# Kernel tuning notes

Measured on AMD Instinct MI355X. Metric: run time of the kernel, lower is better.

The kernel has to match this reference:

```python
import jax, jax.numpy as jnp
import numpy as np

T, R, H, DK = 2, 3, 4, 32
IN_DIM, OUT_DIM = 128, 128
N = 50000
E = 400000
RELS = [(0, 1), (1, 0), (1, 1)]  # (src_type, dst_type) per relation


def setup_inputs() -> dict:
    key = jax.random.key(0)
    ks = jax.random.split(key, 24)
    lin_scale = float(np.sqrt(2.0 / (IN_DIM + OUT_DIM)))
    att_scale = float(np.sqrt(2.0 / (DK + DK)))
    inp = {
        'h0': jax.random.normal(ks[0], (N, IN_DIM), jnp.float32),
        'h1': jax.random.normal(ks[1], (N, IN_DIM), jnp.float32),
        'Wk': jax.random.normal(ks[2], (T, IN_DIM, OUT_DIM), jnp.float32) * lin_scale,
        'bk': jnp.zeros((T, OUT_DIM), jnp.float32),
        'Wq': jax.random.normal(ks[3], (T, IN_DIM, OUT_DIM), jnp.float32) * lin_scale,
        'bq': jnp.zeros((T, OUT_DIM), jnp.float32),
        'Wv': jax.random.normal(ks[4], (T, IN_DIM, OUT_DIM), jnp.float32) * lin_scale,
        'bv': jnp.zeros((T, OUT_DIM), jnp.float32),
        'Wa': jax.random.normal(ks[5], (T, OUT_DIM, OUT_DIM), jnp.float32) * lin_scale,
        'ba': jnp.zeros((T, OUT_DIM), jnp.float32),
        'rel_att': jax.random.normal(ks[6], (R, H, DK, DK), jnp.float32) * att_scale,
        'rel_msg': jax.random.normal(ks[7], (R, H, DK, DK), jnp.float32) * att_scale,
        'rel_pri': jnp.ones((R, H), jnp.float32),
        'skip': jnp.ones((T,), jnp.float32),
        'src0': jax.random.randint(ks[8], (E,), 0, N, jnp.int32),
        'dst0': jax.random.randint(ks[9], (E,), 0, N, jnp.int32),
        'src1': jax.random.randint(ks[10], (E,), 0, N, jnp.int32),
        'dst1': jax.random.randint(ks[11], (E,), 0, N, jnp.int32),
        'src2': jax.random.randint(ks[12], (E,), 0, N, jnp.int32),
        'dst2': jax.random.randint(ks[13], (E,), 0, N, jnp.int32),
    }
    return inp


def _hgt_forward(h0, h1, Wk, bk, Wq, bq, Wv, bv, Wa, ba,
                 rel_att, rel_msg, rel_pri, skip, edges):
    sqrt_dk = np.sqrt(DK).astype(np.float32)
    hs = [h0, h1]
    # per-type k/q/v projections, reshaped to [N, H, DK]
    k_all = [(hs[t] @ Wk[t] + bk[t]).reshape(-1, H, DK) for t in range(T)]
    q_all = [(hs[t] @ Wq[t] + bq[t]).reshape(-1, H, DK) for t in range(T)]
    v_all = [(hs[t] @ Wv[t] + bv[t]).reshape(-1, H, DK) for t in range(T)]
    agg = {0: [], 1: []}
    for r, (s, d) in enumerate(RELS):
        src, dst = edges[r]
        k = jnp.einsum('nhi,hij->nhj', k_all[s], rel_att[r])
        v = jnp.einsum('nhi,hij->nhj', v_all[s], rel_msg[r])
        q = q_all[d]
        # edge-wise dot-product attention score [E, H]
        score = jnp.einsum('ehd,ehd->eh', q[dst], k[src]) * rel_pri[r] / sqrt_dk
        # edge softmax normalized by destination node
        m = jax.ops.segment_max(score, dst, num_segments=N)
        e = jnp.exp(score - m[dst])
        z = jax.ops.segment_sum(e, dst, num_segments=N)
        a = e / z[dst]
        msg = v[src] * a[..., None]  # [E, H, DK]
        agg[d].append(jax.ops.segment_sum(msg, dst, num_segments=N))
    outs = []
    for t in range(T):
        tmean = agg[t][0]
        for extra in agg[t][1:]:
            tmean = tmean + extra
        tmean = tmean / jnp.float32(len(agg[t]))  # cross_reducer='mean'
        tt = tmean.reshape(-1, OUT_DIM)
        trans = tt @ Wa[t] + ba[t]  # dropout p=0 -> identity
        alpha = jax.nn.sigmoid(skip[t])
        outs.append(trans * alpha + hs[t] * (1.0 - alpha))
    return jnp.stack(outs)  # [T, N, OUT_DIM]


def reference(h0, h1, Wk, bk, Wq, bq, Wv, bv, Wa, ba,
              rel_att, rel_msg, rel_pri, skip,
              src0, dst0, src1, dst1, src2, dst2):
    edges = [(src0, dst0), (src1, dst1), (src2, dst2)]
    return _hgt_forward(h0, h1, Wk, bk, Wq, bq, Wv, bv, Wa, ba,
                        rel_att, rel_msg, rel_pri, skip, edges)
```

## Files before the change

### kernel.cpp

```cpp
#include <hip/hip_runtime.h>
#include <hip/hip_bf16.h>
#include <math.h>


#define NN 50000
#define EE 400000
#define CAP 40

typedef __bf16 bf16x8 __attribute__((ext_vector_type(8)));
typedef float floatx4 __attribute__((ext_vector_type(4)));
typedef _Float16 h2 __attribute__((ext_vector_type(2)));

#if __has_builtin(__builtin_amdgcn_exp2f)
#define EXP2F(x) __builtin_amdgcn_exp2f(x)
#else
#define EXP2F(x) exp2f(x)
#endif

__device__ __forceinline__ h2 u_to_h2(unsigned int u) {
    union { unsigned int u; h2 h; } x; x.u = u; return x.h;
}

__device__ __forceinline__ float dot2f(h2 a, h2 b, float c) {
#if __has_builtin(__builtin_amdgcn_fdot2)
    return __builtin_amdgcn_fdot2(a, b, c, false);
#else
    return fmaf((float)a.x, (float)b.x, fmaf((float)a.y, (float)b.y, c));
#endif
}

#define FUSEB 640
#define SCATB 196
__global__ __launch_bounds__(256) void prep(
    const float* __restrict__ Wk, const float* __restrict__ bk,
    const float* __restrict__ Wq, const float* __restrict__ bq,
    const float* __restrict__ Wv, const float* __restrict__ bv,
    const float* __restrict__ rel_att, const float* __restrict__ rel_msg,
    const float* __restrict__ rel_pri, const float* __restrict__ Wa,
    __hip_bfloat16* __restrict__ Wcat0T, __hip_bfloat16* __restrict__ Wcat1T,
    __hip_bfloat16* __restrict__ WaT,
    float* __restrict__ bcat0, float* __restrict__ bcat1,
    const int* __restrict__ s0, const int* __restrict__ d0,
    const int* __restrict__ s1, const int* __restrict__ d1,
    const int* __restrict__ s2, const int* __restrict__ d2,
    int* __restrict__ cursor, int* __restrict__ sorted_src)
{
    if (blockIdx.x >= FUSEB) {
        int sb = blockIdx.x - FUSEB;
        int r = sb / SCATB;
        int blk = sb - r * SCATB;
        const int* S = (r == 0) ? s0 : (r == 1) ? s1 : s2;
        const int* D = (r == 0) ? d0 : (r == 1) ? d1 : d2;
        int e0 = blk * 2048 + threadIdx.x * 8;
        if (e0 + 8 <= EE) {
            int sv[8], dv[8], pos[8];
            *(int4*)&sv[0] = *(const int4*)(S + e0);
            *(int4*)&sv[4] = *(const int4*)(S + e0 + 4);
            *(int4*)&dv[0] = *(const int4*)(D + e0);
            *(int4*)&dv[4] = *(const int4*)(D + e0 + 4);
            #pragma unroll
            for (int j = 0; j < 8; ++j)
                pos[j] = atomicAdd(&cursor[r * NN + dv[j]], 1);
            #pragma unroll
            for (int j = 0; j < 8; ++j)
                if (pos[j] < CAP)
                    sorted_src[(size_t)(r * NN + dv[j]) * CAP + pos[j]] = sv[j];
        } else {
            for (int j = 0; j < 8; ++j) {
                int e = e0 + j;
                if (e >= EE) break;
                int idx = r * NN + D[e];
                int pos = atomicAdd(&cursor[idx], 1);
                if (pos < CAP) sorted_src[(size_t)idx * CAP + pos] = S[e];
            }
        }
        return;
    }
    int idx = blockIdx.x * 256 + threadIdx.x;
    const int R1 = 128 * 384, R2 = 128 * 640, R3 = 2 * 128 * 128;
    if (idx >= R1 + R2 + R3) return;
    if (idx >= R1 + R2) {
        int t = idx - R1 - R2;
        int tt = t >> 14, rem = t & 16383;
        int k = rem >> 7, col = rem & 127;
        WaT[tt * 16384 + col * 128 + k] = __float2bfloat16(Wa[tt * 16384 + k * 128 + col]);
        return;
    }
    int typ, i, col;
    __hip_bfloat16* Wout; float* bout;
    if (idx < R1) { typ = 0; i = idx / 384; col = idx % 384; Wout = Wcat0T; bout = bcat0; }
    else { idx -= R1; typ = 1; i = idx / 640; col = idx % 640; Wout = Wcat1T; bout = bcat1; }
    float w, b;
    if (col < 128) {
        w = Wq[(typ * 128 + i) * 128 + col];
        b = bq[typ * 128 + col];
    } else {
        int kvcol = col - 128;
        int r = (typ == 0) ? 0 : (1 + (kvcol >> 8));
        int gc = kvcol & 255;
        int isV = (gc >> 2) & 1;
        int c = (gc >> 3) * 4 + (gc & 3);
        int s = typ;
        const float* Wsrc = isV ? Wv : Wk;
        const float* bsrc = isV ? bv : bk;
        const float* rel  = isV ? rel_msg : rel_att;
        int h = c >> 5, j = c & 31;
        float acc = 0.f, bacc = 0.f;
        #pragma unroll
        for (int cc = 0; cc < 32; ++cc) {
            float rr = rel[((r * 4 + h) * 32 + cc) * 32 + j];
            acc  += Wsrc[(s * 128 + i) * 128 + h * 32 + cc] * rr;
            bacc += bsrc[s * 128 + h * 32 + cc] * rr;
        }
        if (!isV) {
            float sc = rel_pri[r * 4 + h] * (0.17677669529663687f * 1.4426950408889634f);
            acc *= sc; bacc *= sc;
        }
        w = acc; b = bacc;
    }
    Wout[col * 128 + i] = __float2bfloat16(w);
    if (i == 0) bout[col] = b;
}

__global__ __launch_bounds__(256) void proj_both(
    const float* __restrict__ h0, const float* __restrict__ h1,
    const __hip_bfloat16* __restrict__ W0T, const __hip_bfloat16* __restrict__ W1T,
    const float* __restrict__ b0, const float* __restrict__ b1,
    ushort* __restrict__ Q0, ushort* __restrict__ Q1,
    ushort* __restrict__ KV0, ushort* __restrict__ KV1,
    ushort* __restrict__ KV2)
{
    __shared__ __align__(16) __hip_bfloat16 As[128][136];
    __shared__ __align__(16) ushort Bs[128][136];
    const int tid = threadIdx.x;
    const int row0 = blockIdx.x * 128;
    const int typ = blockIdx.y;
    const float* A = typ ? h1 : h0;
    const __hip_bfloat16* WT = typ ? W1T : W0T;
    const float* bias = typ ? b1 : b0;
    const int ntiles = typ ? 5 : 3;

    #pragma unroll
    for (int it = 0; it < 16; ++it) {
        int li = it * 256 + tid;
        int r = li >> 5, k4 = (li & 31) * 4;
        int grow = row0 + r;
        float4 a4 = make_float4(0.f, 0.f, 0.f, 0.f);
        if (grow < NN) a4 = *(const float4*)(A + (size_t)grow * 128 + k4);
        As[r][k4 + 0] = __float2bfloat16(a4.x);
        As[r][k4 + 1] = __float2bfloat16(a4.y);
        As[r][k4 + 2] = __float2bfloat16(a4.z);
        As[r][k4 + 3] = __float2bfloat16(a4.w);
    }

    const int lane = tid & 63;
    const int wv = tid >> 6;
    const int wr = (wv & 1) * 64, wc = (wv >> 1) * 64;
    const int lr = lane & 15, kq = lane >> 4;

    for (int ct = 0; ct < ntiles; ++ct) {
        __syncthreads();
        #pragma unroll
        for (int it = 0; it < 8; ++it) {
            int li = it * 256 + tid;
            int c = li >> 4, k8 = (li & 15) * 8;
            *(uint4*)&Bs[c][k8] = *(const uint4*)(WT + (size_t)(ct * 128 + c) * 128 + k8);
        }
        __syncthreads();

        floatx4 acc[4][4];
        #pragma unroll
        for (int i = 0; i < 4; ++i)
            #pragma unroll
            for (int j = 0; j < 4; ++j)
                acc[i][j] = (floatx4){0.f, 0.f, 0.f, 0.f};

        #pragma unroll
        for (int kc = 0; kc < 128; kc += 32) {
            bf16x8 a[4], b[4];
            #pragma unroll
            for (int i = 0; i < 4; ++i) a[i] = *(const bf16x8*)&As[wr + i * 16 + lr][kc + kq * 8];
            #pragma unroll
            for (int j = 0; j < 4; ++j) b[j] = *(const bf16x8*)&Bs[wc + j * 16 + lr][kc + kq * 8];
            #pragma unroll
            for (int i = 0; i < 4; ++i)
                #pragma unroll
                for (int j = 0; j < 4; ++j)
                    acc[i][j] = __builtin_amdgcn_mfma_f32_16x16x32_bf16(a[i], b[j], acc[i][j], 0, 0, 0);
        }

        float biasv[4];
        #pragma unroll
        for (int j = 0; j < 4; ++j) biasv[j] = bias[ct * 128 + wc + j * 16 + lr];

        __syncthreads();
        #pragma unroll
        for (int i = 0; i < 4; ++i)
            #pragma unroll
            for (int reg = 0; reg < 4; ++reg) {
                int row = wr + i * 16 + kq * 4 + reg;
                #pragma unroll
                for (int j = 0; j < 4; ++j) {
                    union { _Float16 h; ushort s; } cv;
                    cv.h = (_Float16)(acc[i][j][reg] + biasv[j]);
                    Bs[row][wc + j * 16 + lr] = cv.s;
                }
            }
        __syncthreads();

        ushort* plane; int ld, toff;
        if (ct == 0) { plane = typ ? Q1 : Q0; ld = 128; toff = 0; }
        else {
            int rel = typ ? (1 + ((ct - 1) >> 1)) : 0;
            plane = (rel == 0) ? KV0 : (rel == 1) ? KV1 : KV2;
            ld = 256; toff = ((ct - 1) & 1) * 128;
        }
        #pragma unroll
        for (int it = 0; it < 8; ++it) {
            int li = it * 256 + tid;
            int row = li >> 4, chunk = (li & 15) * 8;
            int grow = row0 + row;
            if (grow < NN)
                *(uint4*)(plane + (size_t)grow * ld + toff + chunk) = *(const uint4*)&Bs[row][chunk];
        }
    }
}

__device__ __forceinline__ void epi_body(
    char* smem,
    const __hip_bfloat16* __restrict__ A0, const __hip_bfloat16* __restrict__ A1, float ascale,
    const __hip_bfloat16* __restrict__ BT, const float* __restrict__ bias,
    float* __restrict__ C, const float* __restrict__ skipGate, const float* __restrict__ Hres)
{
    typedef __hip_bfloat16 bfrow[136];
    bfrow* As = (bfrow*)smem;
    bfrow* Bs = (bfrow*)(smem + 128 * 136 * 2);
    typedef float frow[132];
    frow* St = (frow*)smem;
    const int tid = threadIdx.x;
    const int row0 = blockIdx.x * 128;

    #pragma unroll
    for (int it = 0; it < 8; ++it) {
        int li = it * 256 + tid;
        int c = li >> 4, k8 = (li & 15) * 8;
        *(uint4*)&Bs[c][k8] = *(const uint4*)(BT + (size_t)c * 128 + k8);
    }
    #pragma unroll
    for (int it = 0; it < 8; ++it) {
        int li = it * 256 + tid;
        int r = li >> 4, k8 = (li & 15) * 8;
        int grow = row0 + r;
        __hip_bfloat162 o2[4];
        if (grow < NN) {
            const __hip_bfloat162* pa = (const __hip_bfloat162*)(A0 + (size_t)grow * 128 + k8);
            if (A1) {
                const __hip_bfloat162* pb = (const __hip_bfloat162*)(A1 + (size_t)grow * 128 + k8);
                #pragma unroll
                for (int u = 0; u < 4; ++u) {
                    float2 fa = __bfloat1622float2(pa[u]);
                    float2 fb = __bfloat1622float2(pb[u]);
                    fa.x = (fa.x + fb.x) * ascale;
                    fa.y = (fa.y + fb.y) * ascale;
                    o2[u] = __float22bfloat162_rn(fa);
                }
            } else {
                #pragma unroll
                for (int u = 0; u < 4; ++u) o2[u] = pa[u];
            }
        } else {
            __hip_bfloat162 zz = __float22bfloat162_rn(make_float2(0.f, 0.f));
            #pragma unroll
            for (int u = 0; u < 4; ++u) o2[u] = zz;
        }
        __hip_bfloat162* dst = (__hip_bfloat162*)&As[r][k8];
        #pragma unroll
        for (int u = 0; u < 4; ++u) dst[u] = o2[u];
    }
    __syncthreads();

    const int lane = tid & 63;
    const int wv = tid >> 6;
    const int wr = (wv & 1) * 64, wc = (wv >> 1) * 64;
    const int lr = lane & 15, kq = lane >> 4;

    floatx4 acc[4][4];
    #pragma unroll
    for (int i = 0; i < 4; ++i)
        #pragma unroll
        for (int j = 0; j < 4; ++j)
            acc[i][j] = (floatx4){0.f, 0.f, 0.f, 0.f};

    #pragma unroll
    for (int kc = 0; kc < 128; kc += 32) {
        bf16x8 a[4], b[4];
        #pragma unroll
        for (int i = 0; i < 4; ++i) a[i] = *(const bf16x8*)&As[wr + i * 16 + lr][kc + kq * 8];
        #pragma unroll
        for (int j = 0; j < 4; ++j) b[j] = *(const bf16x8*)&Bs[wc + j * 16 + lr][kc + kq * 8];
        #pragma unroll
        for (int i = 0; i < 4; ++i)
            #pragma unroll
            for (int j = 0; j < 4; ++j)
                acc[i][j] = __builtin_amdgcn_mfma_f32_16x16x32_bf16(a[i], b[j], acc[i][j], 0, 0, 0);
    }

    float sg = *skipGate;
    float alpha = 1.f / (1.f + expf(-sg));
    float beta = 1.f - alpha;
    float biasv[4];
    #pragma unroll
    for (int j = 0; j < 4; ++j) biasv[j] = bias[wc + j * 16 + lr];

    __syncthreads();
    #pragma unroll
    for (int i = 0; i < 4; ++i)
        #pragma unroll
        for (int reg = 0; reg < 4; ++reg) {
            int row = wr + i * 16 + kq * 4 + reg;
            #pragma unroll
            for (int j = 0; j < 4; ++j)
                St[row][wc + j * 16 + lr] = acc[i][j][reg] + biasv[j];
        }
    __syncthreads();

    #pragma unroll
    for (int it = 0; it < 16; ++it) {
        int li = it * 256 + tid;
        int row = li >> 5, chunk = (li & 31) * 4;
        int grow = row0 + row;
        if (grow < NN) {
            float4 v = *(const float4*)&St[row][chunk];
            float4 hr = *(const float4*)(Hres + (size_t)grow * 128 + chunk);
            v.x = v.x * alpha + hr.x * beta;
            v.y = v.y * alpha + hr.y * beta;
            v.z = v.z * alpha + hr.z * beta;
            v.w = v.w * alpha + hr.w * beta;
            *(float4*)(C + (size_t)grow * 128 + chunk) = v;
        }
    }
}

__global__ __launch_bounds__(256) void epi_both(
    const __hip_bfloat16* __restrict__ aggR0, const __hip_bfloat16* __restrict__ aggR1,
    const __hip_bfloat16* __restrict__ aggR2,
    const __hip_bfloat16* __restrict__ WaT, const float* __restrict__ ba,
    float* __restrict__ out, const float* __restrict__ skip,
    const float* __restrict__ h0, const float* __restrict__ h1)
{
    __shared__ __align__(16) char smem[128 * 136 * 2 * 2];
    if (blockIdx.y == 0)
        epi_body(smem, aggR1, nullptr, 1.f, WaT, ba, out, skip, h0);
    else
        epi_body(smem, aggR0, aggR2, 0.5f, WaT + 16384, ba + 128,
                 out + (size_t)NN * 128, skip + 1, h1);
}

__device__ __forceinline__ void edge4_accum(
    uint4 ra, uint4 rb, uint4 rc, uint4 rd,
    bool mA, bool mB, bool mC, bool mD,
    h2 q01, h2 q23,
    float& z, float& u0, float& u1, float& u2, float& u3)
{
    float pa = dot2f(u_to_h2(ra.x), q01, 0.f); pa = dot2f(u_to_h2(ra.y), q23, pa);
    float pb = dot2f(u_to_h2(rb.x), q01, 0.f); pb = dot2f(u_to_h2(rb.y), q23, pb);
    float pc = dot2f(u_to_h2(rc.x), q01, 0.f); pc = dot2f(u_to_h2(rc.y), q23, pc);
    float pd = dot2f(u_to_h2(rd.x), q01, 0.f); pd = dot2f(u_to_h2(rd.y), q23, pd);
    pa += __shfl_xor(pa, 1); pb += __shfl_xor(pb, 1); pc += __shfl_xor(pc, 1); pd += __shfl_xor(pd, 1);
    pa += __shfl_xor(pa, 2); pb += __shfl_xor(pb, 2); pc += __shfl_xor(pc, 2); pd += __shfl_xor(pd, 2);
    pa += __shfl_xor(pa, 4); pb += __shfl_xor(pb, 4); pc += __shfl_xor(pc, 4); pd += __shfl_xor(pd, 4);
    float ea = EXP2F(pa); if (!mA) ea = 0.f;
    float eb = EXP2F(pb); if (!mB) eb = 0.f;
    float ec = EXP2F(pc); if (!mC) ec = 0.f;
    float ed = EXP2F(pd); if (!mD) ed = 0.f;
    z += (ea + eb) + (ec + ed);
    h2 va, vb;
    va = u_to_h2(ra.z); vb = u_to_h2(ra.w);
    u0 = fmaf(ea, (float)va.x, u0); u1 = fmaf(ea, (float)va.y, u1);
    u2 = fmaf(ea, (float)vb.x, u2); u3 = fmaf(ea, (float)vb.y, u3);
    va = u_to_h2(rb.z); vb = u_to_h2(rb.w);
    u0 = fmaf(eb, (float)va.x, u0); u1 = fmaf(eb, (float)va.y, u1);
    u2 = fmaf(eb, (float)vb.x, u2); u3 = fmaf(eb, (float)vb.y, u3);
    va = u_to_h2(rc.z); vb = u_to_h2(rc.w);
    u0 = fmaf(ec, (float)va.x, u0); u1 = fmaf(ec, (float)va.y, u1);
    u2 = fmaf(ec, (float)vb.x, u2); u3 = fmaf(ec, (float)vb.y, u3);
    va = u_to_h2(rd.z); vb = u_to_h2(rd.w);
    u0 = fmaf(ed, (float)va.x, u0); u1 = fmaf(ed, (float)va.y, u1);
    u2 = fmaf(ed, (float)vb.x, u2); u3 = fmaf(ed, (float)vb.y, u3);
}

__global__ __launch_bounds__(256) void aggregate_all(
    const ushort* __restrict__ Q0, const ushort* __restrict__ Q1,
    const ushort* __restrict__ KV0, const ushort* __restrict__ KV1,
    const ushort* __restrict__ KV2,
    const int* __restrict__ sorted, const int* __restrict__ counts,
    __hip_bfloat16* __restrict__ aggR0, __hip_bfloat16* __restrict__ aggR1,
    __hip_bfloat16* __restrict__ aggR2)
{
    int n = (blockIdx.x * 256 + threadIdx.x) >> 6;
    int lane = threadIdx.x & 63;
    int r = blockIdx.y;
    const ushort *Q, *KV; __hip_bfloat16* outp;
    if (r == 0)      { Q = Q1; KV = KV0; outp = aggR0; }
    else if (r == 1) { Q = Q0; KV = KV1; outp = aggR1; }
    else             { Q = Q1; KV = KV2; outp = aggR2; }
    int gw = r * NN + n;

    int hl = lane & 31;
    int half = lane >> 5;
    int cnt = min(counts[gw], CAP);

    if (cnt <= 0) {
        if (half == 0) *(uint2*)(outp + (size_t)n * 128 + hl * 4) = make_uint2(0u, 0u);
        return;
    }

    uint2 qr = *(const uint2*)(Q + (size_t)n * 128 + hl * 4);
    h2 q01 = u_to_h2(qr.x), q23 = u_to_h2(qr.y);
    const int* elist = sorted + (size_t)gw * CAP;
    int4 v0 = *(const int4*)elist;
    int4 v1 = *(const int4*)(elist + 4);

    int ef = v0.x;
    bool mA = (0 + half) < cnt, mB = (2 + half) < cnt, mC = (4 + half) < cnt, mD = (6 + half) < cnt;
    int i0 = mA ? (half ? v0.y : v0.x) : ef;
    int i1 = mB ? (half ? v0.w : v0.z) : ef;
    int i2 = mC ? (half ? v1.y : v1.x) : ef;
    int i3 = mD ? (half ? v1.w : v1.z) : ef;
    uint4 ra = *(const uint4*)(KV + (size_t)(unsigned)(i0 * 256 + hl * 8));
    uint4 rb = *(const uint4*)(KV + (size_t)(unsigned)(i1 * 256 + hl * 8));
    uint4 rc = *(const uint4*)(KV + (size_t)(unsigned)(i2 * 256 + hl * 8));
    uint4 rd = *(const uint4*)(KV + (size_t)(unsigned)(i3 * 256 + hl * 8));

    float u0 = 0.f, u1 = 0.f, u2 = 0.f, u3 = 0.f, z = 0.f;
    edge4_accum(ra, rb, rc, rd, mA, mB, mC, mD, q01, q23, z, u0, u1, u2, u3);

    if (cnt > 8) {
        int4 v2 = *(const int4*)(elist + 8);
        int4 v3 = *(const int4*)(elist + 12);
        bool nA = (8 + half) < cnt, nB = (10 + half) < cnt, nC = (12 + half) < cnt, nD = (14 + half) < cnt;
        int j0 = nA ? (half ? v2.y : v2.x) : ef;
        int j1 = nB ? (half ? v2.w : v2.z) : ef;
        int j2 = nC ? (half ? v3.y : v3.x) : ef;
        int j3 = nD ? (half ? v3.w : v3.z) : ef;
        uint4 sa = *(const uint4*)(KV + (size_t)(unsigned)(j0 * 256 + hl * 8));
        uint4 sb = *(const uint4*)(KV + (size_t)(unsigned)(j1 * 256 + hl * 8));
        uint4 sc = *(const uint4*)(KV + (size_t)(unsigned)(j2 * 256 + hl * 8));
        uint4 sd = *(const uint4*)(KV + (size_t)(unsigned)(j3 * 256 + hl * 8));
        edge4_accum(sa, sb, sc, sd, nA, nB, nC, nD, q01, q23, z, u0, u1, u2, u3);

        for (int i = 16; i < cnt; i += 4) {
            int eA = i + half, eB = i + 2 + half;
            int sA = elist[min(eA, cnt - 1)];
            int sB = elist[min(eB, cnt - 1)];
            uint4 ta = *(const uint4*)(KV + (size_t)(unsigned)(sA * 256 + hl * 8));
            uint4 tb = *(const uint4*)(KV + (size_t)(unsigned)(sB * 256 + hl * 8));
            float pa = dot2f(u_to_h2(ta.x), q01, 0.f); pa = dot2f(u_to_h2(ta.y), q23, pa);
            float pb = dot2f(u_to_h2(tb.x), q01, 0.f); pb = dot2f(u_to_h2(tb.y), q23, pb);
            pa += __shfl_xor(pa, 1); pb += __shfl_xor(pb, 1);
            pa += __shfl_xor(pa, 2); pb += __shfl_xor(pb, 2);
            pa += __shfl_xor(pa, 4); pb += __shfl_xor(pb, 4);
            float ea = EXP2F(pa);
            float eb = EXP2F(pb);
            if (eA >= cnt) ea = 0.f;
            if (eB >= cnt) eb = 0.f;
            z += ea + eb;
            h2 va = u_to_h2(ta.z), vb = u_to_h2(ta.w);
            u0 = fmaf(ea, (float)va.x, u0); u1 = fmaf(ea, (float)va.y, u1);
            u2 = fmaf(ea, (float)vb.x, u2); u3 = fmaf(ea, (float)vb.y, u3);
            va = u_to_h2(tb.z); vb = u_to_h2(tb.w);
            u0 = fmaf(eb, (float)va.x, u0); u1 = fmaf(eb, (float)va.y, u1);
            u2 = fmaf(eb, (float)vb.x, u2); u3 = fmaf(eb, (float)vb.y, u3);
        }
    }

    z  += __shfl_xor(z, 32);
    u0 += __shfl_xor(u0, 32);
    u1 += __shfl_xor(u1, 32);
    u2 += __shfl_xor(u2, 32);
    u3 += __shfl_xor(u3, 32);
    if (half == 0) {
        float inv = 1.f / z;
        __hip_bfloat162 o0 = __float22bfloat162_rn(make_float2(u0 * inv, u1 * inv));
        __hip_bfloat162 o1 = __float22bfloat162_rn(make_float2(u2 * inv, u3 * inv));
        union { uint2 u; __hip_bfloat162 h[2]; } pk2;
        pk2.h[0] = o0; pk2.h[1] = o1;
        *(uint2*)(outp + (size_t)n * 128 + hl * 4) = pk2.u;
    }
}

extern "C" void kernel_launch(void* const* d_in, const int* in_sizes, int n_in,
                              void* d_out, int out_size, void* d_ws, size_t ws_size,
                              hipStream_t stream)
{
    const float* h0      = (const float*)d_in[0];
    const float* h1      = (const float*)d_in[1];
    const float* Wk      = (const float*)d_in[2];
    const float* bk      = (const float*)d_in[3];
    const float* Wq      = (const float*)d_in[4];
    const float* bq      = (const float*)d_in[5];
    const float* Wv      = (const float*)d_in[6];
    const float* bv      = (const float*)d_in[7];
    const float* Wa      = (const float*)d_in[8];
    const float* ba      = (const float*)d_in[9];
    const float* rel_att = (const float*)d_in[10];
    const float* rel_msg = (const float*)d_in[11];
    const float* rel_pri = (const float*)d_in[12];
    const float* skip    = (const float*)d_in[13];
    const int*   src0    = (const int*)d_in[14];
    const int*   dst0    = (const int*)d_in[15];
    const int*   src1    = (const int*)d_in[16];
    const int*   dst1    = (const int*)d_in[17];
    const int*   src2    = (const int*)d_in[18];
    const int*   dst2    = (const int*)d_in[19];
    float* out = (float*)d_out;

    char* w = (char*)d_ws;
    auto alloc = [&](size_t bytes) -> char* {
        char* p = w; w += (bytes + 255) & ~(size_t)255; return p;
    };
    __hip_bfloat16* Wcat0T = (__hip_bfloat16*)alloc(384 * 128 * 2);
    __hip_bfloat16* Wcat1T = (__hip_bfloat16*)alloc(640 * 128 * 2);
    __hip_bfloat16* WaT    = (__hip_bfloat16*)alloc(2 * 128 * 128 * 2);
    float* bcat0 = (float*)alloc(384 * sizeof(float));
    float* bcat1 = (float*)alloc(640 * sizeof(float));
    ushort* Q0  = (ushort*)alloc((size_t)NN * 128 * 2);
    ushort* Q1  = (ushort*)alloc((size_t)NN * 128 * 2);
    ushort* KV0 = (ushort*)alloc((size_t)NN * 256 * 2);
    ushort* KV1 = (ushort*)alloc((size_t)NN * 256 * 2);
    ushort* KV2 = (ushort*)alloc((size_t)NN * 256 * 2);
    __hip_bfloat16* aggR0 = (__hip_bfloat16*)alloc((size_t)NN * 128 * 2);
    __hip_bfloat16* aggR1 = (__hip_bfloat16*)alloc((size_t)NN * 128 * 2);
    __hip_bfloat16* aggR2 = (__hip_bfloat16*)alloc((size_t)NN * 128 * 2);
    int* cursor  = (int*)alloc(3 * NN * sizeof(int));
    int* sorted  = (int*)alloc((size_t)3 * NN * CAP * sizeof(int));

    if ((size_t)(w - (char*)d_ws) > ws_size) return;

    hipMemsetAsync(cursor, 0, 3 * NN * sizeof(int), stream);

    prep<<<FUSEB + 3 * SCATB, 256, 0, stream>>>(
        Wk, bk, Wq, bq, Wv, bv, rel_att, rel_msg, rel_pri, Wa,
        Wcat0T, Wcat1T, WaT, bcat0, bcat1,
        src0, dst0, src1, dst1, src2, dst2, cursor, sorted);

    const int ROWB = (NN + 127) / 128;
    proj_both<<<dim3(ROWB, 2), 256, 0, stream>>>(h0, h1, Wcat0T, Wcat1T, bcat0, bcat1,
                                                 Q0, Q1, KV0, KV1, KV2);

    const int AG = (NN * 64) / 256;
    aggregate_all<<<dim3(AG, 3), 256, 0, stream>>>(Q0, Q1, KV0, KV1, KV2, sorted, cursor,
                                                   aggR0, aggR1, aggR2);

    epi_both<<<dim3(ROWB, 2), 256, 0, stream>>>(aggR0, aggR1, aggR2, WaT, ba, out, skip, h0, h1);
}
```

Before: 370.6 us.

## Issue all 8 initial gathers unconditionally and use DPP/swizzle for lane reductions

The aggregate kernel now loads the first 16 edge indices and issues all eight KV row gathers up front, without data-dependent masking or an early exit. This raises memory-level parallelism. The sorted edge list is zeroed by an enlarged memset so unused slots point at row 0 and stay safe to read. Butterfly reductions for xor 1/2/4 switch from ds_bpermute shuffles to DPP moves and ds_swizzle. The cost is a much larger memset (about 24 MB) and extra gathers for nodes with few edges.

```diff
diff --git a/kernel.cpp b/kernel.cpp
--- a/kernel.cpp
+++ b/kernel.cpp
@@ -26,6 +26,31 @@
     return __builtin_amdgcn_fdot2(a, b, c, false);
 #else
     return fmaf((float)a.x, (float)b.x, fmaf((float)a.y, (float)b.y, c));
+#endif
+}
+
+__device__ __forceinline__ float xor1_add(float x) {
+#if __has_builtin(__builtin_amdgcn_mov_dpp)
+    int y = __builtin_amdgcn_mov_dpp(__float_as_int(x), 0xB1, 0xf, 0xf, true);
+    return x + __int_as_float(y);
+#else
+    return x + __shfl_xor(x, 1);
+#endif
+}
+__device__ __forceinline__ float xor2_add(float x) {
+#if __has_builtin(__builtin_amdgcn_mov_dpp)
+    int y = __builtin_amdgcn_mov_dpp(__float_as_int(x), 0x4E, 0xf, 0xf, true);
+    return x + __int_as_float(y);
+#else
+    return x + __shfl_xor(x, 2);
+#endif
+}
+__device__ __forceinline__ float xor4_add(float x) {
+#if __has_builtin(__builtin_amdgcn_ds_swizzle)
+    int y = __builtin_amdgcn_ds_swizzle(__float_as_int(x), 0x101F);
+    return x + __int_as_float(y);
+#else
+    return x + __shfl_xor(x, 4);
 #endif
 }
 
@@ -366,9 +391,9 @@
     float pb = dot2f(u_to_h2(rb.x), q01, 0.f); pb = dot2f(u_to_h2(rb.y), q23, pb);
     float pc = dot2f(u_to_h2(rc.x), q01, 0.f); pc = dot2f(u_to_h2(rc.y), q23, pc);
     float pd = dot2f(u_to_h2(rd.x), q01, 0.f); pd = dot2f(u_to_h2(rd.y), q23, pd);
-    pa += __shfl_xor(pa, 1); pb += __shfl_xor(pb, 1); pc += __shfl_xor(pc, 1); pd += __shfl_xor(pd, 1);
-    pa += __shfl_xor(pa, 2); pb += __shfl_xor(pb, 2); pc += __shfl_xor(pc, 2); pd += __shfl_xor(pd, 2);
-    pa += __shfl_xor(pa, 4); pb += __shfl_xor(pb, 4); pc += __shfl_xor(pc, 4); pd += __shfl_xor(pd, 4);
+    pa = xor1_add(pa); pb = xor1_add(pb); pc = xor1_add(pc); pd = xor1_add(pd);
+    pa = xor2_add(pa); pb = xor2_add(pb); pc = xor2_add(pc); pd = xor2_add(pd);
+    pa = xor4_add(pa); pb = xor4_add(pb); pc = xor4_add(pc); pd = xor4_add(pd);
     float ea = EXP2F(pa); if (!mA) ea = 0.f;
     float eb = EXP2F(pb); if (!mB) eb = 0.f;
     float ec = EXP2F(pc); if (!mC) ec = 0.f;
@@ -408,45 +433,40 @@
 
     int hl = lane & 31;
     int half = lane >> 5;
+
     int cnt = min(counts[gw], CAP);
-
-    if (cnt <= 0) {
-        if (half == 0) *(uint2*)(outp + (size_t)n * 128 + hl * 4) = make_uint2(0u, 0u);
-        return;
-    }
-
     uint2 qr = *(const uint2*)(Q + (size_t)n * 128 + hl * 4);
-    h2 q01 = u_to_h2(qr.x), q23 = u_to_h2(qr.y);
     const int* elist = sorted + (size_t)gw * CAP;
     int4 v0 = *(const int4*)elist;
     int4 v1 = *(const int4*)(elist + 4);
-
-    int ef = v0.x;
-    bool mA = (0 + half) < cnt, mB = (2 + half) < cnt, mC = (4 + half) < cnt, mD = (6 + half) < cnt;
-    int i0 = mA ? (half ? v0.y : v0.x) : ef;
-    int i1 = mB ? (half ? v0.w : v0.z) : ef;
-    int i2 = mC ? (half ? v1.y : v1.x) : ef;
-    int i3 = mD ? (half ? v1.w : v1.z) : ef;
+    int4 v2 = *(const int4*)(elist + 8);
+    int4 v3 = *(const int4*)(elist + 12);
+
+    int i0 = half ? v0.y : v0.x;
+    int i1 = half ? v0.w : v0.z;
+    int i2 = half ? v1.y : v1.x;
+    int i3 = half ? v1.w : v1.z;
+    int j0 = half ? v2.y : v2.x;
+    int j1 = half ? v2.w : v2.z;
+    int j2 = half ? v3.y : v3.x;
+    int j3 = half ? v3.w : v3.z;
     uint4 ra = *(const uint4*)(KV + (size_t)(unsigned)(i0 * 256 + hl * 8));
     uint4 rb = *(const uint4*)(KV + (size_t)(unsigned)(i1 * 256 + hl * 8));
     uint4 rc = *(const uint4*)(KV + (size_t)(unsigned)(i2 * 256 + hl * 8));
     uint4 rd = *(const uint4*)(KV + (size_t)(unsigned)(i3 * 256 + hl * 8));
-
+    uint4 sa = *(const uint4*)(KV + (size_t)(unsigned)(j0 * 256 + hl * 8));
+    uint4 sb = *(const uint4*)(KV + (size_t)(unsigned)(j1 * 256 + hl * 8));
+    uint4 sc = *(const uint4*)(KV + (size_t)(unsigned)(j2 * 256 + hl * 8));
+    uint4 sd = *(const uint4*)(KV + (size_t)(unsigned)(j3 * 256 + hl * 8));
+
+    h2 q01 = u_to_h2(qr.x), q23 = u_to_h2(qr.y);
+
+    bool mA = (0 + half) < cnt, mB = (2 + half) < cnt, mC = (4 + half) < cnt, mD = (6 + half) < cnt;
     float u0 = 0.f, u1 = 0.f, u2 = 0.f, u3 = 0.f, z = 0.f;
     edge4_accum(ra, rb, rc, rd, mA, mB, mC, mD, q01, q23, z, u0, u1, u2, u3);
 
     if (cnt > 8) {
-        int4 v2 = *(const int4*)(elist + 8);
-        int4 v3 = *(const int4*)(elist + 12);
         bool nA = (8 + half) < cnt, nB = (10 + half) < cnt, nC = (12 + half) < cnt, nD = (14 + half) < cnt;
-        int j0 = nA ? (half ? v2.y : v2.x) : ef;
-        int j1 = nB ? (half ? v2.w : v2.z) : ef;
-        int j2 = nC ? (half ? v3.y : v3.x) : ef;
-        int j3 = nD ? (half ? v3.w : v3.z) : ef;
-        uint4 sa = *(const uint4*)(KV + (size_t)(unsigned)(j0 * 256 + hl * 8));
-        uint4 sb = *(const uint4*)(KV + (size_t)(unsigned)(j1 * 256 + hl * 8));
-        uint4 sc = *(const uint4*)(KV + (size_t)(unsigned)(j2 * 256 + hl * 8));
-        uint4 sd = *(const uint4*)(KV + (size_t)(unsigned)(j3 * 256 + hl * 8));
         edge4_accum(sa, sb, sc, sd, nA, nB, nC, nD, q01, q23, z, u0, u1, u2, u3);
 
         for (int i = 16; i < cnt; i += 4) {
@@ -457,9 +477,9 @@
             uint4 tb = *(const uint4*)(KV + (size_t)(unsigned)(sB * 256 + hl * 8));
             float pa = dot2f(u_to_h2(ta.x), q01, 0.f); pa = dot2f(u_to_h2(ta.y), q23, pa);
             float pb = dot2f(u_to_h2(tb.x), q01, 0.f); pb = dot2f(u_to_h2(tb.y), q23, pb);
-            pa += __shfl_xor(pa, 1); pb += __shfl_xor(pb, 1);
-            pa += __shfl_xor(pa, 2); pb += __shfl_xor(pb, 2);
-            pa += __shfl_xor(pa, 4); pb += __shfl_xor(pb, 4);
+            pa = xor1_add(pa); pb = xor1_add(pb);
+            pa = xor2_add(pa); pb = xor2_add(pb);
+            pa = xor4_add(pa); pb = xor4_add(pb);
             float ea = EXP2F(pa);
             float eb = EXP2F(pb);
             if (eA >= cnt) ea = 0.f;
@@ -480,7 +500,7 @@
     u2 += __shfl_xor(u2, 32);
     u3 += __shfl_xor(u3, 32);
     if (half == 0) {
-        float inv = 1.f / z;
+        float inv = (cnt > 0) ? 1.f / z : 0.f;
         __hip_bfloat162 o0 = __float22bfloat162_rn(make_float2(u0 * inv, u1 * inv));
         __hip_bfloat162 o1 = __float22bfloat162_rn(make_float2(u2 * inv, u3 * inv));
         union { uint2 u; __hip_bfloat162 h[2]; } pk2;
@@ -537,7 +557,8 @@
 
     if ((size_t)(w - (char*)d_ws) > ws_size) return;
 
-    hipMemsetAsync(cursor, 0, 3 * NN * sizeof(int), stream);
+    size_t zlen = (size_t)((char*)sorted - (char*)cursor) + (size_t)3 * NN * CAP * sizeof(int);
+    hipMemsetAsync(cursor, 0, zlen, stream);
 
     prep<<<FUSEB + 3 * SCATB, 256, 0, stream>>>(
         Wk, bk, Wq, bq, Wv, bv, rel_att, rel_msg, rel_pri, Wa,
```

After: 371.4 us. Within noise of the previous version (+0.2%).
